# Kernel optimization log

Measured on AMD Instinct MI355X. Metric: run time of the kernel, lower is better.

The kernel has to match this reference:

```python
import jax, jax.numpy as jnp
import numpy as np
from jax import lax

DIM = 192
HEADS = 8
HIDDEN = int(DIM * 2.66)  # 510
EPS_LN = 1e-5
EPS_NORM = 1e-12


def conv1x1(x, w):
    # x: (B,C,H,W), w: (O,I,1,1)
    return lax.conv_general_dilated(x, w, (1, 1), 'VALID',
                                    dimension_numbers=('NCHW', 'OIHW', 'NCHW'))


def dwconv3x3(x, w):
    # depthwise 3x3, padding=1; w: (C,1,3,3)
    c = x.shape[1]
    return lax.conv_general_dilated(x, w, (1, 1), 'SAME',
                                    dimension_numbers=('NCHW', 'OIHW', 'NCHW'),
                                    feature_group_count=c)


def layernorm_chan(x, weight, bias):
    # WithBias LayerNorm over channel dim of NCHW (matches to_3d -> LN(-1) -> to_4d)
    mu = jnp.mean(x, axis=1, keepdims=True)
    var = jnp.var(x, axis=1, keepdims=True)
    xn = (x - mu) * lax.rsqrt(var + EPS_LN)
    return xn * weight[None, :, None, None] + bias[None, :, None, None]


def l2norm(x):
    # F.normalize along last dim with eps=1e-12
    n = jnp.sqrt(jnp.sum(x * x, axis=-1, keepdims=True))
    return x / jnp.maximum(n, EPS_NORM)


def attention(x, temperature, w_qkv, w_qkv_dw, w_proj):
    b, c, h, w = x.shape
    hw = h * w
    head_dim = c // HEADS
    qkv = dwconv3x3(conv1x1(x, w_qkv), w_qkv_dw)  # (B, 3C, H, W)
    q, k, v = jnp.split(qkv, 3, axis=1)
    q = l2norm(q.reshape(b, HEADS, head_dim, hw))
    k = l2norm(k.reshape(b, HEADS, head_dim, hw))
    v = v.reshape(b, HEADS, head_dim, hw)
    # channel-wise attention: (B,H,d,d)
    attn = jnp.einsum('bhde,bhce->bhdc', q, k) * temperature[None]
    attn = jax.nn.softmax(attn, axis=-1)
    out = jnp.einsum('bhdc,bhce->bhde', attn, v).reshape(b, c, h, w)
    return conv1x1(out, w_proj)


def ffn(x, w_in, w_dw, w_out):
    x = conv1x1(x, w_in)                 # (B, 2*hidden, H, W)
    x = dwconv3x3(x, w_dw)
    x1, x2 = jnp.split(x, 2, axis=1)
    x = jax.nn.gelu(x1, approximate=False) * x2
    return conv1x1(x, w_out)


def setup_inputs() -> dict:
    key = jax.random.key(0)
    ks = jax.random.split(key, 8)
    b, c, h, w = 4, DIM, 128, 128
    s = 0.05
    return {
        'x': jax.random.normal(ks[0], (b, c, h, w), jnp.float32),
        'temperature': jnp.ones((HEADS, 1, 1), jnp.float32),
        'ln1_w': jnp.ones((c,), jnp.float32),
        'ln1_b': jnp.zeros((c,), jnp.float32),
        'ln2_w': jnp.ones((c,), jnp.float32),
        'ln2_b': jnp.zeros((c,), jnp.float32),
        'w_qkv': jax.random.normal(ks[1], (3 * c, c, 1, 1), jnp.float32) * s,
        'w_qkv_dw': jax.random.normal(ks[2], (3 * c, 1, 3, 3), jnp.float32) * s,
        'w_proj': jax.random.normal(ks[3], (c, c, 1, 1), jnp.float32) * s,
        'w_in': jax.random.normal(ks[4], (2 * HIDDEN, c, 1, 1), jnp.float32) * s,
        'w_dw': jax.random.normal(ks[5], (2 * HIDDEN, 1, 3, 3), jnp.float32) * s,
        'w_out_ffn': jax.random.normal(ks[6], (c, HIDDEN, 1, 1), jnp.float32) * s,
    }


def reference(x, temperature, ln1_w, ln1_b, ln2_w, ln2_b, w_qkv, w_qkv_dw,
              w_proj, w_in, w_dw, w_out_ffn):
    x = x + attention(layernorm_chan(x, ln1_w, ln1_b), temperature,
                      w_qkv, w_qkv_dw, w_proj)
    x = x + ffn(layernorm_chan(x, ln2_w, ln2_b), w_in, w_dw, w_out_ffn)
    return x
```

## Files before the change

kernel.cpp:

```cpp
#include <hip/hip_runtime.h>
#include <hip/hip_bf16.h>
#include <math.h>


#define HW_ 16384

typedef __attribute__((ext_vector_type(8))) short bf16x8;
typedef __attribute__((ext_vector_type(4))) float f32x4;
typedef __attribute__((ext_vector_type(16))) float f32x16;
typedef __attribute__((ext_vector_type(4))) int i32x4;

union Pack8 { __hip_bfloat16 h[8]; i32x4 v; };

__global__ __launch_bounds__(256) void convert_weights(
    const float* __restrict__ wqkv, const float* __restrict__ wproj,
    const float* __restrict__ win, const float* __restrict__ wout,
    __hip_bfloat16* __restrict__ oq, __hip_bfloat16* __restrict__ op,
    __hip_bfloat16* __restrict__ oi, __hip_bfloat16* __restrict__ oo) {
  const int i = blockIdx.x * 256 + threadIdx.x;
  if (i < 110592) oq[i] = __float2bfloat16(wqkv[i]);
  if (i < 36864)  op[i] = __float2bfloat16(wproj[i]);
  if (i < 196608) {
    int m = i / 192, k = i - m * 192;
    oi[i] = __float2bfloat16(m < 1020 ? win[m * 192 + k] : 0.f);
  }
  if (i < 98304) {
    int m = i >> 9, k = i & 511;
    oo[i] = __float2bfloat16(k < 510 ? wout[m * 510 + k] : 0.f);
  }
}

__global__ __launch_bounds__(256) void ln_t_kernel(
    const float* __restrict__ x, const float* __restrict__ w,
    const float* __restrict__ bi, __hip_bfloat16* __restrict__ yt) {
  const int b = blockIdx.y;
  x += (size_t)b * 192 * HW_;
  yt += (size_t)b * HW_ * 192;
  __shared__ float tile[192][68];
  __shared__ float psum[4][64], psq[4][64];
  __shared__ float mu_s[64], inv_s[64];
  const int tid = threadIdx.x;
  const int p0 = blockIdx.x * 64;
  for (int idx = tid; idx < 192 * 16; idx += 256) {
    int c = idx >> 4, p4 = idx & 15;
    f32x4 v = *(const f32x4*)(x + (size_t)c * HW_ + p0 + p4 * 4);
    *(f32x4*)&tile[c][p4 * 4] = v;
  }
  __syncthreads();
  const int tx = tid & 63, ty = tid >> 6;
  float s = 0.f, s2 = 0.f;
  for (int c = ty * 48; c < ty * 48 + 48; c++) {
    float v = tile[c][tx]; s += v; s2 += v * v;
  }
  psum[ty][tx] = s; psq[ty][tx] = s2;
  __syncthreads();
  if (ty == 0) {
    float ts = psum[0][tx] + psum[1][tx] + psum[2][tx] + psum[3][tx];
    float ts2 = psq[0][tx] + psq[1][tx] + psq[2][tx] + psq[3][tx];
    float mu = ts * (1.f / 192.f);
    float var = ts2 * (1.f / 192.f) - mu * mu;
    mu_s[tx] = mu; inv_s[tx] = rsqrtf(var + 1e-5f);
  }
  __syncthreads();
  for (int idx = tid; idx < 64 * 24; idx += 256) {
    int c8 = idx % 24, p = idx / 24;
    float mu = mu_s[p], inv = inv_s[p];
    Pack8 pk;
    #pragma unroll
    for (int u = 0; u < 8; u++) {
      int c = c8 * 8 + u;
      pk.h[u] = __float2bfloat16((tile[c][p] - mu) * inv * w[c] + bi[c]);
    }
    *(i32x4*)&yt[(size_t)(p0 + p) * 192 + c8 * 8] = pk.v;
  }
}

template <int EPI>
__global__ __launch_bounds__(256) void gemm_bstat(
    const __hip_bfloat16* __restrict__ A, const __hip_bfloat16* __restrict__ Bg,
    const float* __restrict__ Cres, void* __restrict__ Dout,
    int Mtiles, size_t Bstr, size_t Cstr, size_t Dstr) {
  const int z = blockIdx.y;
  const __hip_bfloat16* B = Bg + (size_t)z * Bstr;
  const int col0 = blockIdx.x * 128;
  __shared__ __align__(16) __hip_bfloat16 Bs[128][192];
  __shared__ __align__(16) __hip_bfloat16 As[64][192];
  const int tid = threadIdx.x;
  const int wave = tid >> 6, lane = tid & 63;
  const int quad = lane >> 4, lr = lane & 15;
  const int wm = (wave & 1) * 32, wn = (wave >> 1) * 64;
  const int lrx = lr & 7;

  const int arow = tid >> 3, ach = tid & 7;
  const int achs = ach ^ (arow & 7);

  #pragma unroll
  for (int l = 0; l < 4; l++) {
    const int row = arow + 32 * l;
    const __hip_bfloat16* bp = B + (size_t)(col0 + row) * 192;
    #pragma unroll
    for (int j = 0; j < 3; j++) {
      i32x4 v = *(const i32x4*)(bp + (ach + 8 * j) * 8);
      *(i32x4*)&Bs[row][(achs + 8 * j) * 8] = v;
    }
  }
  i32x4 areg[6];
  #pragma unroll
  for (int l = 0; l < 2; l++)
    #pragma unroll
    for (int j = 0; j < 3; j++)
      areg[l * 3 + j] = *(const i32x4*)(
          A + (size_t)(arow + 32 * l) * 192 + (ach + 8 * j) * 8);
  #pragma unroll
  for (int l = 0; l < 2; l++)
    #pragma unroll
    for (int j = 0; j < 3; j++)
      *(i32x4*)&As[arow + 32 * l][(achs + 8 * j) * 8] = areg[l * 3 + j];
  __syncthreads();

  for (int mt = 0; mt < Mtiles; mt++) {
    const int row0 = mt * 64;
    if (mt + 1 < Mtiles) {
      const __hip_bfloat16* ap = A + (size_t)(mt + 1) * 64 * 192;
      #pragma unroll
      for (int l = 0; l < 2; l++)
        #pragma unroll
        for (int j = 0; j < 3; j++)
          areg[l * 3 + j] = *(const i32x4*)(
              ap + (size_t)(arow + 32 * l) * 192 + (ach + 8 * j) * 8);
    }
    f32x4 acc[2][4];
    #pragma unroll
    for (int i = 0; i < 2; i++)
      #pragma unroll
      for (int j = 0; j < 4; j++) acc[i][j] = (f32x4){0.f, 0.f, 0.f, 0.f};
    #pragma unroll
    for (int kc = 0; kc < 6; kc++) {
      const int chq = ((kc * 4 + quad) ^ lrx) * 8;
      bf16x8 a0 = *(const bf16x8*)&As[wm + lr][chq];
      bf16x8 a1 = *(const bf16x8*)&As[wm + 16 + lr][chq];
      #pragma unroll
      for (int j = 0; j < 4; j++) {
        bf16x8 bb = *(const bf16x8*)&Bs[wn + j * 16 + lr][chq];
        acc[0][j] = __builtin_amdgcn_mfma_f32_16x16x32_bf16(a0, bb, acc[0][j], 0, 0, 0);
        acc[1][j] = __builtin_amdgcn_mfma_f32_16x16x32_bf16(a1, bb, acc[1][j], 0, 0, 0);
      }
    }
    __syncthreads();
    if (mt + 1 < Mtiles) {
      #pragma unroll
      for (int l = 0; l < 2; l++)
        #pragma unroll
        for (int j = 0; j < 3; j++)
          *(i32x4*)&As[arow + 32 * l][(achs + 8 * j) * 8] = areg[l * 3 + j];
      __syncthreads();
    }
    #pragma unroll
    for (int i = 0; i < 2; i++)
      #pragma unroll
      for (int r = 0; r < 4; r++) {
        const int gm = row0 + wm + i * 16 + quad * 4 + r;
        const size_t base = (size_t)gm * HW_ + col0 + wn + lr;
        if (EPI == 0) {
          __hip_bfloat16* dp = (__hip_bfloat16*)Dout + (size_t)z * Dstr + base;
          #pragma unroll
          for (int j = 0; j < 4; j++) dp[j * 16] = __float2bfloat16(acc[i][j][r]);
        } else {
          float* dp = (float*)Dout + (size_t)z * Dstr + base;
          const float* cp = Cres + (size_t)z * Cstr + base;
          #pragma unroll
          for (int j = 0; j < 4; j++) dp[j * 16] = acc[i][j][r] + cp[j * 16];
        }
      }
  }
}

template <int EPI>
__global__ __launch_bounds__(256) void mfma_gemm(
    const __hip_bfloat16* __restrict__ A, const __hip_bfloat16* __restrict__ Bg,
    const float* __restrict__ Cres, void* __restrict__ Dout,
    int M, int N, int K, size_t Bstr, size_t Cstr, size_t Dstr) {
  const int z = blockIdx.z;
  const __hip_bfloat16* B = Bg + (size_t)z * Bstr;
  const float* C = Cres ? Cres + (size_t)z * Cstr : nullptr;
  __shared__ __align__(16) __hip_bfloat16 As[64][64];
  __shared__ __align__(16) __hip_bfloat16 Bs[128][64];
  const int tid = threadIdx.x;
  const int wave = tid >> 6, lane = tid & 63;
  const int quad = lane >> 4, lr = lane & 15;
  const int lrx = lr & 7;
  const int wm = (wave & 1) * 32, wn = (wave >> 1) * 64;
  const int row0 = blockIdx.x * 64, col0 = blockIdx.y * 128;

  f32x4 acc[2][4];
  #pragma unroll
  for (int i = 0; i < 2; i++)
    #pragma unroll
    for (int j = 0; j < 4; j++) acc[i][j] = (f32x4){0.f, 0.f, 0.f, 0.f};

  for (int k0 = 0; k0 < K; k0 += 64) {
    #pragma unroll
    for (int l = 0; l < 2; l++) {
      int t = tid + l * 256;
      int row = t >> 3, ch = t & 7;
      i32x4 v = *(const i32x4*)(A + (size_t)(row0 + row) * K + k0 + ch * 8);
      *(i32x4*)&As[row][(ch ^ (row & 7)) * 8] = v;
    }
    #pragma unroll
    for (int l = 0; l < 4; l++) {
      int t = tid + l * 256;
      int row = t >> 3, ch = t & 7;
      i32x4 v = *(const i32x4*)(B + (size_t)(col0 + row) * K + k0 + ch * 8);
      *(i32x4*)&Bs[row][(ch ^ (row & 7)) * 8] = v;
    }
    __syncthreads();
    #pragma unroll
    for (int ks = 0; ks < 2; ks++) {
      const int chq = ((ks * 4 + quad) ^ lrx) * 8;
      bf16x8 a0 = *(const bf16x8*)&As[wm + lr][chq];
      bf16x8 a1 = *(const bf16x8*)&As[wm + 16 + lr][chq];
      #pragma unroll
      for (int j = 0; j < 4; j++) {
        bf16x8 bb = *(const bf16x8*)&Bs[wn + j * 16 + lr][chq];
        acc[0][j] = __builtin_amdgcn_mfma_f32_16x16x32_bf16(a0, bb, acc[0][j], 0, 0, 0);
        acc[1][j] = __builtin_amdgcn_mfma_f32_16x16x32_bf16(a1, bb, acc[1][j], 0, 0, 0);
      }
    }
    __syncthreads();
  }

  #pragma unroll
  for (int i = 0; i < 2; i++) {
    #pragma unroll
    for (int r = 0; r < 4; r++) {
      int gm = row0 + wm + i * 16 + quad * 4 + r;
      if (gm >= M) continue;
      #pragma unroll
      for (int j = 0; j < 4; j++) {
        int gn = col0 + wn + j * 16 + lr;
        size_t idx = (size_t)gm * N + gn;
        if (EPI == 0) {
          (((__hip_bfloat16*)Dout) + (size_t)z * Dstr)[idx] = __float2bfloat16(acc[i][j][r]);
        } else {
          (((float*)Dout) + (size_t)z * Dstr)[idx] = acc[i][j][r] + C[idx];
        }
      }
    }
  }
}

__global__ __launch_bounds__(256) void dw_kernel(
    const __hip_bfloat16* __restrict__ in, const float* __restrict__ wdw,
    __hip_bfloat16* __restrict__ out, float* __restrict__ nrm2p) {
  const int b = blockIdx.z;
  in  += (size_t)b * 576 * HW_;
  out += (size_t)b * 576 * HW_;
  const int c = blockIdx.y;
  const int x8 = threadIdx.x & 15;
  const int y = blockIdx.x * 16 + (threadIdx.x >> 4);
  const __hip_bfloat16* ip = in + (size_t)c * HW_;
  const float* wp = wdw + c * 9;
  float wv[9];
  #pragma unroll
  for (int u = 0; u < 9; u++) wv[u] = wp[u];
  i32x4 vrow[3]; float vf[3];
  #pragma unroll
  for (int r = 0; r < 3; r++) {
    const int yy = y + r - 1;
    const int yyc = yy < 0 ? 0 : (yy > 127 ? 127 : yy);
    vf[r] = (yy >= 0 && yy < 128) ? 1.f : 0.f;
    vrow[r] = *(const i32x4*)(ip + yyc * 128 + x8 * 8);
  }
  float acc[8];
  #pragma unroll
  for (int j = 0; j < 8; j++) acc[j] = 0.f;
  #pragma unroll
  for (int r = 0; r < 3; r++) {
    Pack8 mid; mid.v = vrow[r];
    const int hi = vrow[r][3];
    const int lo = vrow[r][0];
    const int lw = __shfl_up(hi, 1, 64);
    const int rw = __shfl_down(lo, 1, 64);
    float row[10];
    row[0] = (x8 > 0) ? vf[r] * (float)(((const __hip_bfloat16*)&lw)[1]) : 0.f;
    #pragma unroll
    for (int u = 0; u < 8; u++) row[1 + u] = vf[r] * (float)mid.h[u];
    row[9] = (x8 < 15) ? vf[r] * (float)(((const __hip_bfloat16*)&rw)[0]) : 0.f;
    const float wl = wv[r * 3], wc = wv[r * 3 + 1], wr = wv[r * 3 + 2];
    #pragma unroll
    for (int j = 0; j < 8; j++)
      acc[j] += wl * row[j] + wc * row[j + 1] + wr * row[j + 2];
  }
  Pack8 o;
  #pragma unroll
  for (int j = 0; j < 8; j++) o.h[j] = __float2bfloat16(acc[j]);
  *(i32x4*)(out + (size_t)c * HW_ + y * 128 + x8 * 8) = o.v;
  if (c < 384) {
    float s = 0.f;
    #pragma unroll
    for (int j = 0; j < 8; j++) s += acc[j] * acc[j];
    #pragma unroll
    for (int off = 32; off > 0; off >>= 1) s += __shfl_down(s, off, 64);
    __shared__ float wsum[4];
    const int lane = threadIdx.x & 63, wvi = threadIdx.x >> 6;
    if (lane == 0) wsum[wvi] = s;
    __syncthreads();
    if (threadIdx.x == 0)
      nrm2p[((size_t)b * 384 + c) * 8 + blockIdx.x] =
          wsum[0] + wsum[1] + wsum[2] + wsum[3];
  }
}

__global__ __launch_bounds__(256) void gram_kernel(
    const __hip_bfloat16* __restrict__ qkv, float* __restrict__ Gpart) {
  const int b = blockIdx.z;
  qkv   += (size_t)b * 576 * HW_;
  Gpart += (size_t)b * 32 * 8 * 576;
  const int h = blockIdx.x, chunk = blockIdx.y;
  const int tid = threadIdx.x;
  const int w = tid >> 6, lane = tid & 63;
  const int m = lane & 31;
  const int khalf = lane >> 5;
  const __hip_bfloat16* qb = qkv + (size_t)(h * 24) * HW_;
  const __hip_bfloat16* kb = qkv + (size_t)(192 + h * 24) * HW_;
  f32x16 acc;
  #pragma unroll
  for (int i = 0; i < 16; i++) acc[i] = 0.f;
  const int e0 = chunk * 512 + w * 128;
  #pragma unroll
  for (int j = 0; j < 8; j++) {
    const int k0 = e0 + j * 16 + khalf * 8;
    bf16x8 a = *(const bf16x8*)(qb + (size_t)m * HW_ + k0);
    bf16x8 bfr = *(const bf16x8*)(kb + (size_t)m * HW_ + k0);
    acc = __builtin_amdgcn_mfma_f32_32x32x16_bf16(a, bfr, acc, 0, 0, 0);
  }
  __shared__ float gs[4][576];
  #pragma unroll
  for (int r = 0; r < 16; r++) {
    int row = (r & 3) + 8 * (r >> 2) + 4 * khalf;
    if (row < 24 && m < 24) gs[w][row * 24 + m] = acc[r];
  }
  __syncthreads();
  float* gp = Gpart + (size_t)(chunk * 8 + h) * 576;
  for (int t = tid; t < 576; t += 256)
    gp[t] = gs[0][t] + gs[1][t] + gs[2][t] + gs[3][t];
}

__global__ __launch_bounds__(256) void softmax2_kernel(
    const float* __restrict__ Gpart, const float* __restrict__ nrm2p,
    const float* __restrict__ temp, float* __restrict__ P) {
  const int b = blockIdx.y;
  Gpart += (size_t)b * 32 * 8 * 576;
  nrm2p += (size_t)b * 384 * 8;
  P     += (size_t)b * 8 * 576;
  const int h = blockIdx.x;
  const int tid = threadIdx.x;
  __shared__ float Gs[576];
  __shared__ float nq[24], nk[24];
  for (int t = tid; t < 576; t += 256) {
    float s = 0.f;
    for (int ch = 0; ch < 32; ch++)
      s += Gpart[(size_t)(ch * 8 + h) * 576 + t];
    Gs[t] = s;
  }
  if (tid < 48) {
    const int r = (tid < 24) ? (h * 24 + tid) : (192 + h * 24 + tid - 24);
    float s = 0.f;
    #pragma unroll
    for (int j = 0; j < 8; j++) s += nrm2p[(size_t)r * 8 + j];
    float nv = fmaxf(sqrtf(s), 1e-12f);
    if (tid < 24) nq[tid] = nv; else nk[tid - 24] = nv;
  }
  __syncthreads();
  if (tid < 24) {
    const int d = tid;
    const float tp = temp[h];
    float row[24], mx = -1e30f;
    #pragma unroll
    for (int c = 0; c < 24; c++) {
      float v = Gs[d * 24 + c] * tp / (nq[d] * nk[c]);
      row[c] = v; mx = fmaxf(mx, v);
    }
    float s = 0.f;
    #pragma unroll
    for (int c = 0; c < 24; c++) { float e = expf(row[c] - mx); row[c] = e; s += e; }
    const float inv = 1.f / s;
    #pragma unroll
    for (int c = 0; c < 24; c++) P[h * 576 + d * 24 + c] = row[c] * inv;
  }
}

__global__ __launch_bounds__(256) void pv_kernel(
    const float* __restrict__ P, const __hip_bfloat16* __restrict__ qkv,
    __hip_bfloat16* __restrict__ yt) {
  const int b = blockIdx.z;
  P   += (size_t)b * 8 * 576;
  qkv += (size_t)b * 576 * HW_;
  yt  += (size_t)b * HW_ * 192;
  const int hh = blockIdx.x;
  const int e = blockIdx.y * 256 + threadIdx.x;
  __shared__ float Ps[576];
  for (int t = threadIdx.x; t < 576; t += 256) Ps[t] = P[hh * 576 + t];
  __syncthreads();
  const __hip_bfloat16* vb = qkv + (size_t)(384 + hh * 24) * HW_;
  float acc[24];
  #pragma unroll
  for (int d = 0; d < 24; d++) acc[d] = 0.f;
  for (int c = 0; c < 24; c++) {
    float v = (float)vb[(size_t)c * HW_ + e];
    #pragma unroll
    for (int d = 0; d < 24; d++) acc[d] += Ps[d * 24 + c] * v;
  }
  #pragma unroll
  for (int g = 0; g < 3; g++) {
    Pack8 pk;
    #pragma unroll
    for (int u = 0; u < 8; u++) pk.h[u] = __float2bfloat16(acc[g * 8 + u]);
    *(i32x4*)&yt[(size_t)e * 192 + hh * 24 + g * 8] = pk.v;
  }
}

__global__ __launch_bounds__(256) void dwg_t_kernel(
    const __hip_bfloat16* __restrict__ hsrc, const float* __restrict__ wdw,
    __hip_bfloat16* __restrict__ gt, int b0) {
  const int z = blockIdx.z;
  const int bb = b0 + z;
  const int yt = blockIdx.x >> 1, xh = blockIdx.x & 1;
  const int cz = blockIdx.y;
  const int tid = threadIdx.x;
  const int cl = tid >> 3, x8 = tid & 7;
  const int c = cz * 32 + cl;
  const int y0 = yt * 4;
  const int pxb = xh * 64 + x8 * 8;
  __shared__ __hip_bfloat16 sg[32][266];

  const bool active = (c < 510);
  const int ca = active ? c : 0;
  const __hip_bfloat16* ha = hsrc + ((size_t)bb * 1024 + ca) * HW_;
  const __hip_bfloat16* hb = hsrc + ((size_t)bb * 1024 + ca + 510) * HW_;
  float wva[9], wvb[9];
  #pragma unroll
  for (int u = 0; u < 9; u++) {
    wva[u] = active ? wdw[c * 9 + u] : 0.f;
    wvb[u] = active ? wdw[(c + 510) * 9 + u] : 0.f;
  }

  i32x4 va[6], vbv[6];
  float vf[6];
  int offr[6];
  #pragma unroll
  for (int i = 0; i < 6; i++) {
    const int ry = y0 - 1 + i;
    const int ryc = ry < 0 ? 0 : (ry > 127 ? 127 : ry);
    vf[i] = (ry >= 0 && ry < 128) ? 1.f : 0.f;
    offr[i] = ryc * 128 + pxb;
    va[i]  = *(const i32x4*)(ha + offr[i]);
    vbv[i] = *(const i32x4*)(hb + offr[i]);
  }
  float leA[6], leB[6], reA[6], reB[6];
  #pragma unroll
  for (int i = 0; i < 6; i++) { leA[i] = 0.f; leB[i] = 0.f; reA[i] = 0.f; reB[i] = 0.f; }
  if (x8 == 0 && xh == 1) {
    #pragma unroll
    for (int i = 0; i < 6; i++) {
      leA[i] = vf[i] * (float)ha[offr[i] - 1];
      leB[i] = vf[i] * (float)hb[offr[i] - 1];
    }
  }
  if (x8 == 7 && xh == 0) {
    #pragma unroll
    for (int i = 0; i < 6; i++) {
      reA[i] = vf[i] * (float)ha[offr[i] + 8];
      reB[i] = vf[i] * (float)hb[offr[i] + 8];
    }
  }

  float aA[3][8], aB[3][8];
  #pragma unroll
  for (int s = 0; s < 3; s++)
    #pragma unroll
    for (int j = 0; j < 8; j++) { aA[s][j] = 0.f; aB[s][j] = 0.f; }

  #pragma unroll
  for (int i = 0; i < 6; i++) {
    const int hiA = va[i][3],  loA = va[i][0];
    const int hiB = vbv[i][3], loB = vbv[i][0];
    const int lwA = __shfl_up(hiA, 1, 64), rwA = __shfl_down(loA, 1, 64);
    const int lwB = __shfl_up(hiB, 1, 64), rwB = __shfl_down(loB, 1, 64);
    Pack8 ma; ma.v = va[i];
    Pack8 mb; mb.v = vbv[i];
    float ra[10], rb[10];
    ra[0] = (x8 > 0) ? vf[i] * (float)(((const __hip_bfloat16*)&lwA)[1]) : leA[i];
    rb[0] = (x8 > 0) ? vf[i] * (float)(((const __hip_bfloat16*)&lwB)[1]) : leB[i];
    #pragma unroll
    for (int u = 0; u < 8; u++) {
      ra[1 + u] = vf[i] * (float)ma.h[u];
      rb[1 + u] = vf[i] * (float)mb.h[u];
    }
    ra[9] = (x8 < 7) ? vf[i] * (float)(((const __hip_bfloat16*)&rwA)[0]) : reA[i];
    rb[9] = (x8 < 7) ? vf[i] * (float)(((const __hip_bfloat16*)&rwB)[0]) : reB[i];
    #pragma unroll
    for (int r = 0; r < 3; r++) {
      const int lo = i - r;
      if (lo < 0 || lo >= 4) continue;
      const int s = lo % 3;
      const float a0 = wva[r * 3], a1 = wva[r * 3 + 1], a2 = wva[r * 3 + 2];
      const float b0w = wvb[r * 3], b1 = wvb[r * 3 + 1], b2 = wvb[r * 3 + 2];
      #pragma unroll
      for (int j = 0; j < 8; j++) {
        aA[s][j] += a0 * ra[j] + a1 * ra[j + 1] + a2 * ra[j + 2];
        aB[s][j] += b0w * rb[j] + b1 * rb[j + 1] + b2 * rb[j + 2];
      }
    }
    {
      const int lo = i - 2;
      if (lo >= 0 && lo < 4) {
        const int s = lo % 3;
        Pack8 o;
        #pragma unroll
        for (int j = 0; j < 8; j++) {
          float v = aA[s][j];
          float ge = 0.5f * v * (1.f + erff(v * 0.70710678118654752f));
          o.h[j] = __float2bfloat16(ge * aB[s][j]);
          aA[s][j] = 0.f; aB[s][j] = 0.f;
        }
        *(i32x4*)&sg[cl][lo * 64 + x8 * 8] = o.v;
      }
    }
  }
  __syncthreads();
  const int sp = tid >> 2, ch0 = (tid & 3) * 8;
  #pragma unroll
  for (int k = 0; k < 4; k++) {
    Pack8 o;
    #pragma unroll
    for (int u = 0; u < 8; u++) o.h[u] = sg[ch0 + u][k * 64 + sp];
    const int gp = (y0 + k) * 128 + xh * 64 + sp;
    *(i32x4*)&gt[((size_t)z * HW_ + gp) * 512 + cz * 32 + ch0] = o.v;
  }
}

extern "C" void kernel_launch(void* const* d_in, const int* in_sizes, int n_in,
                              void* d_out, int out_size, void* d_ws, size_t ws_size,
                              hipStream_t stream) {
  const float* x     = (const float*)d_in[0];
  const float* temp  = (const float*)d_in[1];
  const float* ln1w  = (const float*)d_in[2];
  const float* ln1b  = (const float*)d_in[3];
  const float* ln2w  = (const float*)d_in[4];
  const float* ln2b  = (const float*)d_in[5];
  const float* wqkv  = (const float*)d_in[6];
  const float* wqkvdw= (const float*)d_in[7];
  const float* wproj = (const float*)d_in[8];
  const float* win   = (const float*)d_in[9];
  const float* wdw   = (const float*)d_in[10];
  const float* wout  = (const float*)d_in[11];
  float* out = (float*)d_out;
  char* ws = (char*)d_ws;

  const int HW = 16384;
  const size_t HWC = (size_t)192 * HW;

  __hip_bfloat16* yt    = (__hip_bfloat16*)(ws + 0);
  __hip_bfloat16* qkva  = (__hip_bfloat16*)(ws + 25165824);
  __hip_bfloat16* qkvb  = (__hip_bfloat16*)(ws + 100663296);
  __hip_bfloat16* hbuf  = (__hip_bfloat16*)(ws + 25165824);
  float*          xa    = (float*)(ws + 176160768);
  __hip_bfloat16* gt    = (__hip_bfloat16*)(ws + 226492416);
  __hip_bfloat16* wqkvB = (__hip_bfloat16*)(ws + 260046848);
  __hip_bfloat16* wprojB= (__hip_bfloat16*)(ws + 260268032);
  __hip_bfloat16* winB  = (__hip_bfloat16*)(ws + 260341760);
  __hip_bfloat16* woutB = (__hip_bfloat16*)(ws + 260734976);
  float*          nrm2p = (float*)(ws + 260931584);
  float*          Gpart = (float*)(ws + 260980736);
  float*          P     = (float*)(ws + 263340032);

  convert_weights<<<768, 256, 0, stream>>>(wqkv, wproj, win, wout,
                                           wqkvB, wprojB, winB, woutB);

  ln_t_kernel<<<dim3(256, 4), 256, 0, stream>>>(x, ln1w, ln1b, yt);
  gemm_bstat<0><<<dim3(128, 4), 256, 0, stream>>>(
      wqkvB, yt, nullptr, qkva, 9, (size_t)HW * 192, 0, (size_t)576 * HW);
  dw_kernel<<<dim3(8, 576, 4), 256, 0, stream>>>(qkva, wqkvdw, qkvb, nrm2p);
  gram_kernel<<<dim3(8, 32, 4), 256, 0, stream>>>(qkvb, Gpart);
  softmax2_kernel<<<dim3(8, 4), 256, 0, stream>>>(Gpart, nrm2p, temp, P);
  pv_kernel<<<dim3(8, 64, 4), 256, 0, stream>>>(P, qkvb, yt);
  gemm_bstat<1><<<dim3(128, 4), 256, 0, stream>>>(
      wprojB, yt, x, xa, 3, (size_t)HW * 192, HWC, HWC);
  ln_t_kernel<<<dim3(256, 4), 256, 0, stream>>>(xa, ln2w, ln2b, yt);
  gemm_bstat<0><<<dim3(128, 4), 256, 0, stream>>>(
      winB, yt, nullptr, hbuf, 16, (size_t)HW * 192, 0, (size_t)1024 * HW);
  for (int half = 0; half < 2; half++) {
    const int b0 = half * 2;
    dwg_t_kernel<<<dim3(64, 16, 2), 256, 0, stream>>>(hbuf, wdw, gt, b0);
    mfma_gemm<1><<<dim3(3, 128, 2), 256, 0, stream>>>(
        woutB, gt, xa + (size_t)b0 * HWC, out + (size_t)b0 * HWC,
        192, HW, 512, (size_t)HW * 512, HWC, HWC);
  }
}
```

Measured before the change: 461.3 us.

## Specialize output GEMM to full-M tiles and overlap A-tile refill with epilogue

Replaces the generic mfma_gemm used for the FFN output projection with gemm_wout. Each block now covers all 192 output rows and 64 columns, so every gt column tile is read once instead of once per M-tile (three times before), and the K, M and N sizes are fixed at compile time. In gemm_bstat, the refill of the next A tile into shared memory moves after the epilogue stores, which may let global stores overlap that work. The larger A tile (192x64) raises shared-memory use and register pressure (24 accumulators), which could lower occupancy.

Result: slower. 499.9 us (+8.4%).

```diff
diff --git a/kernel.cpp b/kernel.cpp
--- a/kernel.cpp
+++ b/kernel.cpp
@@ -146,15 +146,6 @@
         acc[1][j] = __builtin_amdgcn_mfma_f32_16x16x32_bf16(a1, bb, acc[1][j], 0, 0, 0);
       }
     }
-    __syncthreads();
-    if (mt + 1 < Mtiles) {
-      #pragma unroll
-      for (int l = 0; l < 2; l++)
-        #pragma unroll
-        for (int j = 0; j < 3; j++)
-          *(i32x4*)&As[arow + 32 * l][(achs + 8 * j) * 8] = areg[l * 3 + j];
-      __syncthreads();
-    }
     #pragma unroll
     for (int i = 0; i < 2; i++)
       #pragma unroll
@@ -172,81 +163,81 @@
           for (int j = 0; j < 4; j++) dp[j * 16] = acc[i][j][r] + cp[j * 16];
         }
       }
-  }
-}
-
-template <int EPI>
-__global__ __launch_bounds__(256) void mfma_gemm(
+    __syncthreads();
+    if (mt + 1 < Mtiles) {
+      #pragma unroll
+      for (int l = 0; l < 2; l++)
+        #pragma unroll
+        for (int j = 0; j < 3; j++)
+          *(i32x4*)&As[arow + 32 * l][(achs + 8 * j) * 8] = areg[l * 3 + j];
+      __syncthreads();
+    }
+  }
+}
+
+__global__ __launch_bounds__(256) void gemm_wout(
     const __hip_bfloat16* __restrict__ A, const __hip_bfloat16* __restrict__ Bg,
-    const float* __restrict__ Cres, void* __restrict__ Dout,
-    int M, int N, int K, size_t Bstr, size_t Cstr, size_t Dstr) {
-  const int z = blockIdx.z;
-  const __hip_bfloat16* B = Bg + (size_t)z * Bstr;
-  const float* C = Cres ? Cres + (size_t)z * Cstr : nullptr;
-  __shared__ __align__(16) __hip_bfloat16 As[64][64];
-  __shared__ __align__(16) __hip_bfloat16 Bs[128][64];
+    const float* __restrict__ Cres, float* __restrict__ Dout) {
+  const int z = blockIdx.y;
+  const __hip_bfloat16* B = Bg + (size_t)z * HW_ * 512;
+  const float* C = Cres + (size_t)z * 192 * HW_;
+  float* D = Dout + (size_t)z * 192 * HW_;
+  const int col0 = blockIdx.x * 64;
+  __shared__ __align__(16) __hip_bfloat16 As[192][64];
+  __shared__ __align__(16) __hip_bfloat16 Bs[64][64];
   const int tid = threadIdx.x;
   const int wave = tid >> 6, lane = tid & 63;
   const int quad = lane >> 4, lr = lane & 15;
   const int lrx = lr & 7;
-  const int wm = (wave & 1) * 32, wn = (wave >> 1) * 64;
-  const int row0 = blockIdx.x * 64, col0 = blockIdx.y * 128;
-
-  f32x4 acc[2][4];
-  #pragma unroll
-  for (int i = 0; i < 2; i++)
-    #pragma unroll
-    for (int j = 0; j < 4; j++) acc[i][j] = (f32x4){0.f, 0.f, 0.f, 0.f};
-
-  for (int k0 = 0; k0 < K; k0 += 64) {
+  const int wm = (wave & 1) * 96, wn = (wave >> 1) * 32;
+
+  f32x4 acc[6][2];
+  #pragma unroll
+  for (int f = 0; f < 6; f++)
+    #pragma unroll
+    for (int j = 0; j < 2; j++) acc[f][j] = (f32x4){0.f, 0.f, 0.f, 0.f};
+
+  for (int k0 = 0; k0 < 512; k0 += 64) {
+    #pragma unroll
+    for (int l = 0; l < 6; l++) {
+      const int t = tid + l * 256;
+      const int row = t >> 3, ch = t & 7;
+      i32x4 v = *(const i32x4*)(A + (size_t)row * 512 + k0 + ch * 8);
+      *(i32x4*)&As[row][(ch ^ (row & 7)) * 8] = v;
+    }
     #pragma unroll
     for (int l = 0; l < 2; l++) {
-      int t = tid + l * 256;
-      int row = t >> 3, ch = t & 7;
-      i32x4 v = *(const i32x4*)(A + (size_t)(row0 + row) * K + k0 + ch * 8);
-      *(i32x4*)&As[row][(ch ^ (row & 7)) * 8] = v;
-    }
-    #pragma unroll
-    for (int l = 0; l < 4; l++) {
-      int t = tid + l * 256;
-      int row = t >> 3, ch = t & 7;
-      i32x4 v = *(const i32x4*)(B + (size_t)(col0 + row) * K + k0 + ch * 8);
+      const int t = tid + l * 256;
+      const int row = t >> 3, ch = t & 7;
+      i32x4 v = *(const i32x4*)(B + (size_t)(col0 + row) * 512 + k0 + ch * 8);
       *(i32x4*)&Bs[row][(ch ^ (row & 7)) * 8] = v;
     }
     __syncthreads();
     #pragma unroll
     for (int ks = 0; ks < 2; ks++) {
       const int chq = ((ks * 4 + quad) ^ lrx) * 8;
-      bf16x8 a0 = *(const bf16x8*)&As[wm + lr][chq];
-      bf16x8 a1 = *(const bf16x8*)&As[wm + 16 + lr][chq];
-      #pragma unroll
-      for (int j = 0; j < 4; j++) {
-        bf16x8 bb = *(const bf16x8*)&Bs[wn + j * 16 + lr][chq];
-        acc[0][j] = __builtin_amdgcn_mfma_f32_16x16x32_bf16(a0, bb, acc[0][j], 0, 0, 0);
-        acc[1][j] = __builtin_amdgcn_mfma_f32_16x16x32_bf16(a1, bb, acc[1][j], 0, 0, 0);
+      bf16x8 b0 = *(const bf16x8*)&Bs[wn + lr][chq];
+      bf16x8 b1 = *(const bf16x8*)&Bs[wn + 16 + lr][chq];
+      #pragma unroll
+      for (int f = 0; f < 6; f++) {
+        bf16x8 aa = *(const bf16x8*)&As[wm + f * 16 + lr][chq];
+        acc[f][0] = __builtin_amdgcn_mfma_f32_16x16x32_bf16(aa, b0, acc[f][0], 0, 0, 0);
+        acc[f][1] = __builtin_amdgcn_mfma_f32_16x16x32_bf16(aa, b1, acc[f][1], 0, 0, 0);
       }
     }
     __syncthreads();
   }
-
-  #pragma unroll
-  for (int i = 0; i < 2; i++) {
+  #pragma unroll
+  for (int f = 0; f < 6; f++)
     #pragma unroll
     for (int r = 0; r < 4; r++) {
-      int gm = row0 + wm + i * 16 + quad * 4 + r;
-      if (gm >= M) continue;
-      #pragma unroll
-      for (int j = 0; j < 4; j++) {
-        int gn = col0 + wn + j * 16 + lr;
-        size_t idx = (size_t)gm * N + gn;
-        if (EPI == 0) {
-          (((__hip_bfloat16*)Dout) + (size_t)z * Dstr)[idx] = __float2bfloat16(acc[i][j][r]);
-        } else {
-          (((float*)Dout) + (size_t)z * Dstr)[idx] = acc[i][j][r] + C[idx];
-        }
+      const int gm = wm + f * 16 + quad * 4 + r;
+      #pragma unroll
+      for (int j = 0; j < 2; j++) {
+        const size_t idx = (size_t)gm * HW_ + col0 + wn + j * 16 + lr;
+        D[idx] = acc[f][j][r] + C[idx];
       }
     }
-  }
 }
 
 __global__ __launch_bounds__(256) void dw_kernel(
@@ -593,8 +584,7 @@
   for (int half = 0; half < 2; half++) {
     const int b0 = half * 2;
     dwg_t_kernel<<<dim3(64, 16, 2), 256, 0, stream>>>(hbuf, wdw, gt, b0);
-    mfma_gemm<1><<<dim3(3, 128, 2), 256, 0, stream>>>(
-        woutB, gt, xa + (size_t)b0 * HWC, out + (size_t)b0 * HWC,
-        192, HW, 512, (size_t)HW * 512, HWC, HWC);
-  }
-}
+    gemm_wout<<<dim3(256, 2), 256, 0, stream>>>(
+        woutB, gt, xa + (size_t)b0 * HWC, out + (size_t)b0 * HWC);
+  }
+}
```
